# Kernel optimization log

Hardware: AMD Instinct MI355X
Metric: run time of the kernel (lower is better)

## Reference

```python
import jax, jax.numpy as jnp
import numpy as np

N = 100000      # nodes
E = 1600000     # edges (avg degree 16)
DIN = 128       # in_feats
H = 4           # num_heads
D = 32          # out_feats per head
NEG_SLOPE = 0.2


def setup_inputs() -> dict:
    key = jax.random.key(0)
    k1, k2, k3, k4, k5, k6 = jax.random.split(key, 6)
    feat = jax.random.normal(k1, (N, DIN), dtype=jnp.float32)
    src = jax.random.randint(k2, (E,), 0, N, dtype=jnp.int32)
    dst = jax.random.randint(k3, (E,), 0, N, dtype=jnp.int32)
    # learned params (fc kernel + attention vectors)
    W = jax.random.normal(k4, (DIN, H * D), dtype=jnp.float32) * 0.05
    attn_l = jax.random.normal(k5, (H, D), dtype=jnp.float32) * 0.05
    attn_r = jax.random.normal(k6, (H, D), dtype=jnp.float32) * 0.05
    return {"feat": feat, "src": src, "dst": dst, "W": W,
            "attn_l": attn_l, "attn_r": attn_r}


def reference(feat, src, dst, W, attn_l, attn_r):
    # linear projection: (N, DIN) @ (DIN, H*D) -> (N, H, D)
    h = (feat @ W).reshape(N, H, D)
    # per-node attention half-logits: (N, H)
    el = jnp.einsum("nhd,hd->nh", h, attn_l)
    er = jnp.einsum("nhd,hd->nh", h, attn_r)
    # edge-wise logits e_ij = LeakyReLU(el[src] + er[dst]) : (E, H)
    e = jax.nn.leaky_relu(el[src] + er[dst], negative_slope=NEG_SLOPE)
    # segment softmax over incoming edges of each dst node
    emax = jax.ops.segment_max(e, dst, num_segments=N)          # (N, H)
    emax = jnp.where(jnp.isfinite(emax), emax, 0.0)             # empty segs
    ee = jnp.exp(e - emax[dst])                                 # (E, H)
    denom = jax.ops.segment_sum(ee, dst, num_segments=N)        # (N, H)
    a = ee / denom[dst]                                         # (E, H)
    # weighted message + scatter-sum aggregation: (N, H, D)
    msg = h[src] * a[:, :, None]                                # (E, H, D)
    out = jax.ops.segment_sum(msg, dst, num_segments=N)
    return out
```

## Files before the change

kernel.cpp:

```cpp
#include <hip/hip_runtime.h>
#include <hip/hip_fp16.h>

#define N_NODES 100000
#define N_EDGES 1600000
#define DIN 128
#define NH 4
#define ND 32
#define HD 128
#define NEG_SLOPE 0.2f
#define MROWS 64
#define APAD 136
#define GEMM_BLOCKS ((N_NODES + MROWS - 1) / MROWS)

#define NBUCK 782
#define CHB 6400
#define NHB 250
#define WCONV_BLOCKS 64

typedef _Float16 half8_t __attribute__((ext_vector_type(8)));
typedef float f32x4 __attribute__((ext_vector_type(4)));

__device__ __forceinline__ float lrelu(float x) {
    return x > 0.0f ? x : NEG_SLOPE * x;
}

union Pack8  { uint2 u; __half2 h2[2]; };
union Pack16 { uint4 u; __half2 h2[4]; };

__global__ __launch_bounds__(256) void k_histw(
    const int* __restrict__ dst, int* __restrict__ hist,
    const float* __restrict__ W, __half* __restrict__ Wt) {
    __shared__ int cnt[NBUCK];
    const int tid = threadIdx.x;

    if ((int)blockIdx.x >= NHB) {
        int i = (blockIdx.x - NHB) * 256 + tid;
        int k = i >> 7, c = i & 127;
        Wt[c * DIN + k] = __float2half(W[k * HD + c]);
        return;
    }
    if (!hist) return;
    for (int i = tid; i < NBUCK; i += 256) cnt[i] = 0;
    __syncthreads();
    int base = blockIdx.x * CHB;
#pragma unroll
    for (int j = 0; j < CHB / 256; ++j) {
        int e = base + j * 256 + tid;
        if (e < N_EDGES) atomicAdd(&cnt[dst[e] >> 7], 1);
    }
    __syncthreads();
    int* hrow = hist + (size_t)blockIdx.x * NBUCK;
    for (int i = tid; i < NBUCK; i += 256) hrow[i] = cnt[i];
}

__global__ __launch_bounds__(256) void k_scanH(int* __restrict__ hist,
                                               int* __restrict__ tot) {
    __shared__ int wtot[4];
    int b = blockIdx.x, tid = threadIdx.x;
    int v = (tid < NHB) ? hist[(size_t)tid * NBUCK + b] : 0;
    int lane = tid & 63, wv = tid >> 6;
    int incl = v;
#pragma unroll
    for (int off = 1; off < 64; off <<= 1) {
        int t = __shfl_up(incl, off, 64);
        if (lane >= off) incl += t;
    }
    if (lane == 63) wtot[wv] = incl;
    __syncthreads();
    int woff = 0;
    for (int w = 0; w < wv; ++w) woff += wtot[w];
    if (tid < NHB) hist[(size_t)tid * NBUCK + b] = woff + incl - v;
    if (tid == 0) tot[b] = wtot[0] + wtot[1] + wtot[2] + wtot[3];
}

__global__ __launch_bounds__(256) void k_scanT(const int* __restrict__ tot,
                                               int* __restrict__ bucket_base,
                                               int* __restrict__ rowptr) {
    __shared__ int wtot[4];
    int tid = threadIdx.x;
    int idx0 = tid * 4;
    int v[4];
#pragma unroll
    for (int j = 0; j < 4; ++j) {
        int b = idx0 + j;
        v[j] = (b < NBUCK) ? tot[b] : 0;
    }
    int s = v[0] + v[1] + v[2] + v[3];
    int lane = tid & 63;
    int incl = s;
#pragma unroll
    for (int off = 1; off < 64; off <<= 1) {
        int t = __shfl_up(incl, off, 64);
        if (lane >= off) incl += t;
    }
    if (lane == 63) wtot[tid >> 6] = incl;
    __syncthreads();
    int woff = 0;
    for (int w = 0; w < (tid >> 6); ++w) woff += wtot[w];
    int run = woff + incl - s;
#pragma unroll
    for (int j = 0; j < 4; ++j) {
        int b = idx0 + j;
        if (b < NBUCK) {
            int old = v[j];
            bucket_base[b] = run;
            run += old;
        }
    }
    if (tid == 0) {
        int total = wtot[0] + wtot[1] + wtot[2] + wtot[3];
        bucket_base[NBUCK] = total;
        rowptr[N_NODES] = total;
    }
}

__global__ __launch_bounds__(256) void k_gemmcscat(
    const float* __restrict__ feat, const __half* __restrict__ Wt,
    const float* __restrict__ attn_l, const float* __restrict__ attn_r,
    __half* __restrict__ hhalf, float* __restrict__ el, float* __restrict__ er,
    const int* __restrict__ src, const int* __restrict__ dst,
    const int* __restrict__ hist, const int* __restrict__ bucket_base,
    int* __restrict__ bucketed) {

    __shared__ __align__(16) __half As[MROWS * APAD];
    __shared__ __align__(16) __half Bs[HD * APAD];

    const int tid = threadIdx.x;

    if ((int)blockIdx.x < NHB) {
        if (!bucketed) return;
        int* cur = (int*)As;
        const int* hrow = hist + (size_t)blockIdx.x * NBUCK;
        for (int i = tid; i < NBUCK; i += 256) cur[i] = bucket_base[i] + hrow[i];
        __syncthreads();
        int base = blockIdx.x * CHB;
#pragma unroll
        for (int j = 0; j < CHB / 256; ++j) {
            int e = base + j * 256 + tid;
            if (e < N_EDGES) {
                int d = dst[e];
                int slot = atomicAdd(&cur[d >> 7], 1);
                bucketed[slot] = src[e] | ((d & 127) << 17);
            }
        }
        return;
    }

    const int row0 = (blockIdx.x - NHB) * MROWS;

    {
        const uint4* Wv = (const uint4*)Wt;
#pragma unroll
        for (int i = 0; i < 8; ++i) {
            int idx = tid + i * 256;
            int c = idx >> 4, k8 = idx & 15;
            *(uint4*)(&Bs[c * APAD + k8 * 8]) = Wv[idx];
        }
    }
    {
#pragma unroll
        for (int i = 0; i < 8; ++i) {
            int idx = tid + i * 256;
            int r = idx >> 5, c4 = idx & 31;
            int row = row0 + r;
            float4 f = (row < N_NODES)
                ? *(const float4*)(feat + (size_t)row * DIN + c4 * 4)
                : make_float4(0.0f, 0.0f, 0.0f, 0.0f);
            Pack8 pk;
            pk.h2[0] = __floats2half2_rn(f.x, f.y);
            pk.h2[1] = __floats2half2_rn(f.z, f.w);
            *(uint2*)(&As[r * APAD + c4 * 4]) = pk.u;
        }
    }
    __syncthreads();

    const int l = tid & 63;
    const int wv = tid >> 6;
    const int lrow = l & 15;
    const int kid = l >> 4;

    f32x4 acc[8];
#pragma unroll
    for (int n = 0; n < 8; ++n) acc[n] = (f32x4){0.0f, 0.0f, 0.0f, 0.0f};

#pragma unroll
    for (int kb = 0; kb < 4; ++kb) {
        half8_t a = *(const half8_t*)(&As[(wv * 16 + lrow) * APAD + kb * 32 + kid * 8]);
#pragma unroll
        for (int n = 0; n < 8; ++n) {
            half8_t b = *(const half8_t*)(&Bs[(n * 16 + lrow) * APAD + kb * 32 + kid * 8]);
            acc[n] = __builtin_amdgcn_mfma_f32_16x16x32_f16(a, b, acc[n], 0, 0, 0);
        }
    }

    __syncthreads();
#pragma unroll
    for (int n = 0; n < 8; ++n)
#pragma unroll
        for (int r = 0; r < 4; ++r)
            As[(wv * 16 + kid * 4 + r) * APAD + n * 16 + lrow] =
                __float2half(acc[n][r]);
    __syncthreads();

    {
        int lr = tid >> 2;
        int row = row0 + lr;
        int head = tid & 3;
        if (row < N_NODES) {
            float suml = 0.0f, sumr = 0.0f;
#pragma unroll
            for (int q = 0; q < 4; ++q) {
                Pack16 p;
                p.u = *(const uint4*)(&As[lr * APAD + head * 32 + q * 8]);
                float4 al0 = *(const float4*)(attn_l + head * 32 + q * 8);
                float4 al1 = *(const float4*)(attn_l + head * 32 + q * 8 + 4);
                float4 ar0 = *(const float4*)(attn_r + head * 32 + q * 8);
                float4 ar1 = *(const float4*)(attn_r + head * 32 + q * 8 + 4);
                float2 x0 = __half22float2(p.h2[0]);
                float2 x1 = __half22float2(p.h2[1]);
                float2 x2 = __half22float2(p.h2[2]);
                float2 x3 = __half22float2(p.h2[3]);
                suml += x0.x * al0.x + x0.y * al0.y + x1.x * al0.z + x1.y * al0.w;
                suml += x2.x * al1.x + x2.y * al1.y + x3.x * al1.z + x3.y * al1.w;
                sumr += x0.x * ar0.x + x0.y * ar0.y + x1.x * ar0.z + x1.y * ar0.w;
                sumr += x2.x * ar1.x + x2.y * ar1.y + x3.x * ar1.z + x3.y * ar1.w;
                *(uint4*)(hhalf + (size_t)row * HD + head * 32 + q * 8) = p.u;
            }
            el[(size_t)row * NH + head] = suml;
            er[(size_t)row * NH + head] = sumr;
        }
    }
}

__global__ __launch_bounds__(512) void k_fine(
    const int* __restrict__ bucketed, const int* __restrict__ bbase,
    int* __restrict__ srcs, int* __restrict__ rowptr) {

    __shared__ int cnt[128];
    __shared__ int noff[129];
    __shared__ int cur[128];

    const int b = blockIdx.x;
    const int tid = threadIdx.x;
    const int node0 = b << 7;
    const int beg = bbase[b], end = bbase[b + 1];

    if (tid < 128) cnt[tid] = 0;
    __syncthreads();

    for (int e = beg + tid; e < end; e += 512)
        atomicAdd(&cnt[bucketed[e] >> 17], 1);
    __syncthreads();

    if (tid < 64) {
        int v0 = cnt[tid * 2], v1 = cnt[tid * 2 + 1];
        int s = v0 + v1;
        int incl = s;
#pragma unroll
        for (int off = 1; off < 64; off <<= 1) {
            int t = __shfl_up(incl, off, 64);
            if (tid >= off) incl += t;
        }
        int excl = incl - s;
        noff[tid * 2] = excl;
        noff[tid * 2 + 1] = excl + v0;
        cur[tid * 2] = excl;
        cur[tid * 2 + 1] = excl + v0;
        if (tid == 63) noff[128] = incl;
    }
    __syncthreads();

    if (tid < 128) {
        int node = node0 + tid;
        if (node < N_NODES) rowptr[node] = beg + noff[tid];
    }

    for (int e = beg + tid; e < end; e += 512) {
        int p = bucketed[e];
        int d7 = p >> 17;
        int slot = beg + atomicAdd(&cur[d7], 1);
        srcs[slot] = p & 0x1FFFF;
    }
}

__global__ __launch_bounds__(256) void k_agg_csr(
    const int* __restrict__ rowptr, const int* __restrict__ srcs,
    const float* __restrict__ el, const float* __restrict__ er,
    const __half* __restrict__ hhalf, float* __restrict__ out) {
    int node = blockIdx.x * 4 + (threadIdx.x >> 6);
    int lane = threadIdx.x & 63;
    int grp = lane >> 4;
    int cl = lane & 15;
    int head = cl >> 2;
    int beg = rowptr[node], end = rowptr[node + 1];

    const float er_h = er[(size_t)node * NH + head];

    float dsum = 0.0f;
    float a[8];
#pragma unroll
    for (int q = 0; q < 8; ++q) a[q] = 0.0f;

    int i = beg + grp;
    for (; i + 12 < end; i += 16) {
        int s0 = srcs[i], s1 = srcs[i + 4], s2 = srcs[i + 8], s3 = srcs[i + 12];
        float e0 = el[(size_t)s0 * NH + head];
        float e1 = el[(size_t)s1 * NH + head];
        float e2 = el[(size_t)s2 * NH + head];
        float e3 = el[(size_t)s3 * NH + head];
        Pack16 p0, p1, p2, p3;
        p0.u = *(const uint4*)(hhalf + (size_t)s0 * HD + cl * 8);
        p1.u = *(const uint4*)(hhalf + (size_t)s1 * HD + cl * 8);
        p2.u = *(const uint4*)(hhalf + (size_t)s2 * HD + cl * 8);
        p3.u = *(const uint4*)(hhalf + (size_t)s3 * HD + cl * 8);
        float w0 = __expf(lrelu(e0 + er_h));
        float w1 = __expf(lrelu(e1 + er_h));
        float w2 = __expf(lrelu(e2 + er_h));
        float w3 = __expf(lrelu(e3 + er_h));
        dsum += (w0 + w1) + (w2 + w3);
#pragma unroll
        for (int q = 0; q < 4; ++q) {
            float2 x0 = __half22float2(p0.h2[q]);
            float2 x1 = __half22float2(p1.h2[q]);
            float2 x2 = __half22float2(p2.h2[q]);
            float2 x3 = __half22float2(p3.h2[q]);
            a[2 * q]     = fmaf(x0.x, w0, a[2 * q]);
            a[2 * q + 1] = fmaf(x0.y, w0, a[2 * q + 1]);
            a[2 * q]     = fmaf(x1.x, w1, a[2 * q]);
            a[2 * q + 1] = fmaf(x1.y, w1, a[2 * q + 1]);
            a[2 * q]     = fmaf(x2.x, w2, a[2 * q]);
            a[2 * q + 1] = fmaf(x2.y, w2, a[2 * q + 1]);
            a[2 * q]     = fmaf(x3.x, w3, a[2 * q]);
            a[2 * q + 1] = fmaf(x3.y, w3, a[2 * q + 1]);
        }
    }
    for (; i + 4 < end; i += 8) {
        int s0 = srcs[i], s1 = srcs[i + 4];
        float e0 = el[(size_t)s0 * NH + head];
        float e1 = el[(size_t)s1 * NH + head];
        Pack16 p0, p1;
        p0.u = *(const uint4*)(hhalf + (size_t)s0 * HD + cl * 8);
        p1.u = *(const uint4*)(hhalf + (size_t)s1 * HD + cl * 8);
        float w0 = __expf(lrelu(e0 + er_h));
        float w1 = __expf(lrelu(e1 + er_h));
        dsum += w0 + w1;
#pragma unroll
        for (int q = 0; q < 4; ++q) {
            float2 x0 = __half22float2(p0.h2[q]);
            float2 x1 = __half22float2(p1.h2[q]);
            a[2 * q]     = fmaf(x0.x, w0, a[2 * q]);
            a[2 * q + 1] = fmaf(x0.y, w0, a[2 * q + 1]);
            a[2 * q]     = fmaf(x1.x, w1, a[2 * q]);
            a[2 * q + 1] = fmaf(x1.y, w1, a[2 * q + 1]);
        }
    }
    if (i < end) {
        int s0 = srcs[i];
        float w0 = __expf(lrelu(el[(size_t)s0 * NH + head] + er_h));
        Pack16 p0;
        p0.u = *(const uint4*)(hhalf + (size_t)s0 * HD + cl * 8);
        dsum += w0;
#pragma unroll
        for (int q = 0; q < 4; ++q) {
            float2 x0 = __half22float2(p0.h2[q]);
            a[2 * q]     = fmaf(x0.x, w0, a[2 * q]);
            a[2 * q + 1] = fmaf(x0.y, w0, a[2 * q + 1]);
        }
    }

    dsum += __shfl_xor(dsum, 16, 64);
    dsum += __shfl_xor(dsum, 32, 64);
#pragma unroll
    for (int q = 0; q < 8; ++q) {
        a[q] += __shfl_xor(a[q], 16, 64);
        a[q] += __shfl_xor(a[q], 32, 64);
    }

    if (grp == 0) {
        float inv = (end > beg) ? 1.0f / dsum : 0.0f;
        *(float4*)(out + (size_t)node * HD + cl * 8) =
            make_float4(a[0] * inv, a[1] * inv, a[2] * inv, a[3] * inv);
        *(float4*)(out + (size_t)node * HD + cl * 8 + 4) =
            make_float4(a[4] * inv, a[5] * inv, a[6] * inv, a[7] * inv);
    }
}

__global__ void k_init_fb(float* __restrict__ out, float* __restrict__ denom) {
    int i = blockIdx.x * blockDim.x + threadIdx.x;
    int stride = gridDim.x * blockDim.x;
    for (int j = i; j < N_NODES * HD; j += stride) out[j] = 0.0f;
    for (int j = i; j < N_NODES * NH; j += stride) denom[j] = 0.0f;
}

__global__ __launch_bounds__(256) void k_denom_fb(
    const int* __restrict__ src, const int* __restrict__ dst,
    const float* __restrict__ el, const float* __restrict__ er,
    float* __restrict__ denom) {
    int e = blockIdx.x * blockDim.x + threadIdx.x;
    if (e >= N_EDGES) return;
    int s = src[e], d = dst[e];
    float4 l = *(const float4*)(el + (size_t)s * NH);
    float4 r = *(const float4*)(er + (size_t)d * NH);
    float* dn = denom + (size_t)d * NH;
    atomicAdd(dn + 0, __expf(lrelu(l.x + r.x)));
    atomicAdd(dn + 1, __expf(lrelu(l.y + r.y)));
    atomicAdd(dn + 2, __expf(lrelu(l.z + r.z)));
    atomicAdd(dn + 3, __expf(lrelu(l.w + r.w)));
}

__global__ __launch_bounds__(256) void k_agg_fb(
    const int* __restrict__ src, const int* __restrict__ dst,
    const float* __restrict__ el, const float* __restrict__ er,
    const float* __restrict__ denom, const __half* __restrict__ hhalf,
    float* __restrict__ out) {
    long long t = (long long)blockIdx.x * blockDim.x + threadIdx.x;
    if (t >= (long long)N_EDGES * HD) return;
    int e = (int)(t >> 7);
    int c = (int)(t & 127);
    int hh = c >> 5;
    int s = src[e], d = dst[e];
    float x = lrelu(el[(size_t)s * NH + hh] + er[(size_t)d * NH + hh]);
    float a = __expf(x) / denom[(size_t)d * NH + hh];
    atomicAdd(out + (size_t)d * HD + c,
              __half2float(hhalf[(size_t)s * HD + c]) * a);
}

extern "C" void kernel_launch(void* const* d_in, const int* in_sizes, int n_in,
                              void* d_out, int out_size, void* d_ws, size_t ws_size,
                              hipStream_t stream) {
    const float* feat   = (const float*)d_in[0];
    const int*   src    = (const int*)d_in[1];
    const int*   dst    = (const int*)d_in[2];
    const float* W      = (const float*)d_in[3];
    const float* attn_l = (const float*)d_in[4];
    const float* attn_r = (const float*)d_in[5];
    float* out = (float*)d_out;

    char* base = (char*)d_ws;
    size_t off = 0;
    auto take = [&](size_t bytes) -> char* {
        char* r = base + off;
        off = (off + bytes + 255) & ~(size_t)255;
        return r;
    };
    __half* hhalf  = (__half*)take((size_t)N_NODES * HD * 2);
    float* el      = (float*)take((size_t)N_NODES * NH * 4);
    float* er      = (float*)take((size_t)N_NODES * NH * 4);
    __half* Wt     = (__half*)take((size_t)DIN * HD * 2);
    int*  hist     = (int*)take((size_t)NHB * NBUCK * 4);
    int*  tot      = (int*)take((size_t)NBUCK * 4);
    int*  bbase    = (int*)take((size_t)(NBUCK + 1) * 4);
    int*  bucketed = (int*)take((size_t)N_EDGES * 4);
    int*  srcs     = (int*)take((size_t)N_EDGES * 4);
    int*  rowptr   = (int*)take((size_t)(N_NODES + 1) * 4);
    float* denom   = (float*)take((size_t)N_NODES * NH * 4);
    bool csr = (off <= ws_size);

    if (csr) {
        k_histw<<<NHB + WCONV_BLOCKS, 256, 0, stream>>>(dst, hist, W, Wt);
        k_scanH<<<NBUCK, 256, 0, stream>>>(hist, tot);
        k_scanT<<<1, 256, 0, stream>>>(tot, bbase, rowptr);
        k_gemmcscat<<<NHB + GEMM_BLOCKS, 256, 0, stream>>>(
            feat, Wt, attn_l, attn_r, hhalf, el, er,
            src, dst, hist, bbase, bucketed);
        k_fine<<<NBUCK, 512, 0, stream>>>(bucketed, bbase, srcs, rowptr);
        k_agg_csr<<<N_NODES / 4, 256, 0, stream>>>(rowptr, srcs, el, er,
                                                   hhalf, out);
    } else {
        int eb = (N_EDGES + 255) / 256;
        k_init_fb<<<2048, 256, 0, stream>>>(out, denom);
        k_histw<<<NHB + WCONV_BLOCKS, 256, 0, stream>>>(dst, (int*)nullptr,
                                                        W, Wt);
        k_gemmcscat<<<NHB + GEMM_BLOCKS, 256, 0, stream>>>(
            feat, Wt, attn_l, attn_r, hhalf, el, er,
            src, dst, (const int*)nullptr, (const int*)nullptr, (int*)nullptr);
        k_denom_fb<<<eb, 256, 0, stream>>>(src, dst, el, er, denom);
        long long totw = (long long)N_EDGES * HD;
        int ab = (int)((totw + 255) / 256);
        k_agg_fb<<<ab, 256, 0, stream>>>(src, dst, el, er, denom, hhalf, out);
    }
}
```

Measured before the change: 147.0 us.

## Split GEMM tiles across scatter and fine-sort kernels to overlap work

Moves the projection GEMM tile code into a shared device function and splits the GEMM blocks between two launches. The first 800 tiles run alongside the coarse bucket scatter, and the remaining tiles run in a new fused kernel alongside the fine per-node sort, whose blocks shrink from 512 to 256 threads. The aim is to balance the load and fill the GPU in both phases instead of running a GEMM-heavy kernel followed by a lighter sort kernel. The risk is that 256-thread sort blocks run more slowly, and the shared-memory footprint of the fused kernel could reduce occupancy.

```diff
diff --git a/kernel.cpp b/kernel.cpp
--- a/kernel.cpp
+++ b/kernel.cpp
@@ -11,6 +11,7 @@
 #define MROWS 64
 #define APAD 136
 #define GEMM_BLOCKS ((N_NODES + MROWS - 1) / MROWS)
+#define G1SPLIT 800
 
 #define NBUCK 782
 #define CHB 6400
@@ -27,126 +28,11 @@
 union Pack8  { uint2 u; __half2 h2[2]; };
 union Pack16 { uint4 u; __half2 h2[4]; };
 
-__global__ __launch_bounds__(256) void k_histw(
-    const int* __restrict__ dst, int* __restrict__ hist,
-    const float* __restrict__ W, __half* __restrict__ Wt) {
-    __shared__ int cnt[NBUCK];
-    const int tid = threadIdx.x;
-
-    if ((int)blockIdx.x >= NHB) {
-        int i = (blockIdx.x - NHB) * 256 + tid;
-        int k = i >> 7, c = i & 127;
-        Wt[c * DIN + k] = __float2half(W[k * HD + c]);
-        return;
-    }
-    if (!hist) return;
-    for (int i = tid; i < NBUCK; i += 256) cnt[i] = 0;
-    __syncthreads();
-    int base = blockIdx.x * CHB;
-#pragma unroll
-    for (int j = 0; j < CHB / 256; ++j) {
-        int e = base + j * 256 + tid;
-        if (e < N_EDGES) atomicAdd(&cnt[dst[e] >> 7], 1);
-    }
-    __syncthreads();
-    int* hrow = hist + (size_t)blockIdx.x * NBUCK;
-    for (int i = tid; i < NBUCK; i += 256) hrow[i] = cnt[i];
-}
-
-__global__ __launch_bounds__(256) void k_scanH(int* __restrict__ hist,
-                                               int* __restrict__ tot) {
-    __shared__ int wtot[4];
-    int b = blockIdx.x, tid = threadIdx.x;
-    int v = (tid < NHB) ? hist[(size_t)tid * NBUCK + b] : 0;
-    int lane = tid & 63, wv = tid >> 6;
-    int incl = v;
-#pragma unroll
-    for (int off = 1; off < 64; off <<= 1) {
-        int t = __shfl_up(incl, off, 64);
-        if (lane >= off) incl += t;
-    }
-    if (lane == 63) wtot[wv] = incl;
-    __syncthreads();
-    int woff = 0;
-    for (int w = 0; w < wv; ++w) woff += wtot[w];
-    if (tid < NHB) hist[(size_t)tid * NBUCK + b] = woff + incl - v;
-    if (tid == 0) tot[b] = wtot[0] + wtot[1] + wtot[2] + wtot[3];
-}
-
-__global__ __launch_bounds__(256) void k_scanT(const int* __restrict__ tot,
-                                               int* __restrict__ bucket_base,
-                                               int* __restrict__ rowptr) {
-    __shared__ int wtot[4];
-    int tid = threadIdx.x;
-    int idx0 = tid * 4;
-    int v[4];
-#pragma unroll
-    for (int j = 0; j < 4; ++j) {
-        int b = idx0 + j;
-        v[j] = (b < NBUCK) ? tot[b] : 0;
-    }
-    int s = v[0] + v[1] + v[2] + v[3];
-    int lane = tid & 63;
-    int incl = s;
-#pragma unroll
-    for (int off = 1; off < 64; off <<= 1) {
-        int t = __shfl_up(incl, off, 64);
-        if (lane >= off) incl += t;
-    }
-    if (lane == 63) wtot[tid >> 6] = incl;
-    __syncthreads();
-    int woff = 0;
-    for (int w = 0; w < (tid >> 6); ++w) woff += wtot[w];
-    int run = woff + incl - s;
-#pragma unroll
-    for (int j = 0; j < 4; ++j) {
-        int b = idx0 + j;
-        if (b < NBUCK) {
-            int old = v[j];
-            bucket_base[b] = run;
-            run += old;
-        }
-    }
-    if (tid == 0) {
-        int total = wtot[0] + wtot[1] + wtot[2] + wtot[3];
-        bucket_base[NBUCK] = total;
-        rowptr[N_NODES] = total;
-    }
-}
-
-__global__ __launch_bounds__(256) void k_gemmcscat(
-    const float* __restrict__ feat, const __half* __restrict__ Wt,
+__device__ __forceinline__ void gemm_tile(
+    int row0, const float* __restrict__ feat, const __half* __restrict__ Wt,
     const float* __restrict__ attn_l, const float* __restrict__ attn_r,
     __half* __restrict__ hhalf, float* __restrict__ el, float* __restrict__ er,
-    const int* __restrict__ src, const int* __restrict__ dst,
-    const int* __restrict__ hist, const int* __restrict__ bucket_base,
-    int* __restrict__ bucketed) {
-
-    __shared__ __align__(16) __half As[MROWS * APAD];
-    __shared__ __align__(16) __half Bs[HD * APAD];
-
-    const int tid = threadIdx.x;
-
-    if ((int)blockIdx.x < NHB) {
-        if (!bucketed) return;
-        int* cur = (int*)As;
-        const int* hrow = hist + (size_t)blockIdx.x * NBUCK;
-        for (int i = tid; i < NBUCK; i += 256) cur[i] = bucket_base[i] + hrow[i];
-        __syncthreads();
-        int base = blockIdx.x * CHB;
-#pragma unroll
-        for (int j = 0; j < CHB / 256; ++j) {
-            int e = base + j * 256 + tid;
-            if (e < N_EDGES) {
-                int d = dst[e];
-                int slot = atomicAdd(&cur[d >> 7], 1);
-                bucketed[slot] = src[e] | ((d & 127) << 17);
-            }
-        }
-        return;
-    }
-
-    const int row0 = (blockIdx.x - NHB) * MROWS;
+    __half* As, __half* Bs, int tid) {
 
     {
         const uint4* Wv = (const uint4*)Wt;
@@ -232,55 +118,191 @@
     }
 }
 
-__global__ __launch_bounds__(512) void k_fine(
+__global__ __launch_bounds__(256) void k_histw(
+    const int* __restrict__ dst, int* __restrict__ hist,
+    const float* __restrict__ W, __half* __restrict__ Wt) {
+    __shared__ int cnt[NBUCK];
+    const int tid = threadIdx.x;
+
+    if ((int)blockIdx.x >= NHB) {
+        int i = (blockIdx.x - NHB) * 256 + tid;
+        int k = i >> 7, c = i & 127;
+        Wt[c * DIN + k] = __float2half(W[k * HD + c]);
+        return;
+    }
+    if (!hist) return;
+    for (int i = tid; i < NBUCK; i += 256) cnt[i] = 0;
+    __syncthreads();
+    int base = blockIdx.x * CHB;
+#pragma unroll
+    for (int j = 0; j < CHB / 256; ++j) {
+        int e = base + j * 256 + tid;
+        if (e < N_EDGES) atomicAdd(&cnt[dst[e] >> 7], 1);
+    }
+    __syncthreads();
+    int* hrow = hist + (size_t)blockIdx.x * NBUCK;
+    for (int i = tid; i < NBUCK; i += 256) hrow[i] = cnt[i];
+}
+
+__global__ __launch_bounds__(256) void k_scanH(int* __restrict__ hist,
+                                               int* __restrict__ tot) {
+    __shared__ int wtot[4];
+    int b = blockIdx.x, tid = threadIdx.x;
+    int v = (tid < NHB) ? hist[(size_t)tid * NBUCK + b] : 0;
+    int lane = tid & 63, wv = tid >> 6;
+    int incl = v;
+#pragma unroll
+    for (int off = 1; off < 64; off <<= 1) {
+        int t = __shfl_up(incl, off, 64);
+        if (lane >= off) incl += t;
+    }
+    if (lane == 63) wtot[wv] = incl;
+    __syncthreads();
+    int woff = 0;
+    for (int w = 0; w < wv; ++w) woff += wtot[w];
+    if (tid < NHB) hist[(size_t)tid * NBUCK + b] = woff + incl - v;
+    if (tid == 0) tot[b] = wtot[0] + wtot[1] + wtot[2] + wtot[3];
+}
+
+__global__ __launch_bounds__(256) void k_scanT(const int* __restrict__ tot,
+                                               int* __restrict__ bucket_base,
+                                               int* __restrict__ rowptr) {
+    __shared__ int wtot[4];
+    int tid = threadIdx.x;
+    int idx0 = tid * 4;
+    int v[4];
+#pragma unroll
+    for (int j = 0; j < 4; ++j) {
+        int b = idx0 + j;
+        v[j] = (b < NBUCK) ? tot[b] : 0;
+    }
+    int s = v[0] + v[1] + v[2] + v[3];
+    int lane = tid & 63;
+    int incl = s;
+#pragma unroll
+    for (int off = 1; off < 64; off <<= 1) {
+        int t = __shfl_up(incl, off, 64);
+        if (lane >= off) incl += t;
+    }
+    if (lane == 63) wtot[tid >> 6] = incl;
+    __syncthreads();
+    int woff = 0;
+    for (int w = 0; w < (tid >> 6); ++w) woff += wtot[w];
+    int run = woff + incl - s;
+#pragma unroll
+    for (int j = 0; j < 4; ++j) {
+        int b = idx0 + j;
+        if (b < NBUCK) {
+            int old = v[j];
+            bucket_base[b] = run;
+            run += old;
+        }
+    }
+    if (tid == 0) {
+        int total = wtot[0] + wtot[1] + wtot[2] + wtot[3];
+        bucket_base[NBUCK] = total;
+        rowptr[N_NODES] = total;
+    }
+}
+
+__global__ __launch_bounds__(256) void k_gemmcscat(
+    const float* __restrict__ feat, const __half* __restrict__ Wt,
+    const float* __restrict__ attn_l, const float* __restrict__ attn_r,
+    __half* __restrict__ hhalf, float* __restrict__ el, float* __restrict__ er,
+    const int* __restrict__ src, const int* __restrict__ dst,
+    const int* __restrict__ hist, const int* __restrict__ bucket_base,
+    int* __restrict__ bucketed) {
+
+    __shared__ __align__(16) __half As[MROWS * APAD];
+    __shared__ __align__(16) __half Bs[HD * APAD];
+
+    const int tid = threadIdx.x;
+
+    if ((int)blockIdx.x < NHB) {
+        if (!bucketed) return;
+        int* cur = (int*)As;
+        const int* hrow = hist + (size_t)blockIdx.x * NBUCK;
+        for (int i = tid; i < NBUCK; i += 256) cur[i] = bucket_base[i] + hrow[i];
+        __syncthreads();
+        int base = blockIdx.x * CHB;
+#pragma unroll
+        for (int j = 0; j < CHB / 256; ++j) {
+            int e = base + j * 256 + tid;
+            if (e < N_EDGES) {
+                int d = dst[e];
+                int slot = atomicAdd(&cur[d >> 7], 1);
+                bucketed[slot] = src[e] | ((d & 127) << 17);
+            }
+        }
+        return;
+    }
+
+    gemm_tile((blockIdx.x - NHB) * MROWS, feat, Wt, attn_l, attn_r,
+              hhalf, el, er, As, Bs, tid);
+}
+
+__global__ __launch_bounds__(256) void k_gemmfine(
+    const float* __restrict__ feat, const __half* __restrict__ Wt,
+    const float* __restrict__ attn_l, const float* __restrict__ attn_r,
+    __half* __restrict__ hhalf, float* __restrict__ el, float* __restrict__ er,
     const int* __restrict__ bucketed, const int* __restrict__ bbase,
     int* __restrict__ srcs, int* __restrict__ rowptr) {
 
-    __shared__ int cnt[128];
-    __shared__ int noff[129];
-    __shared__ int cur[128];
-
-    const int b = blockIdx.x;
+    __shared__ __align__(16) __half As[MROWS * APAD];
+    __shared__ __align__(16) __half Bs[HD * APAD];
+
     const int tid = threadIdx.x;
-    const int node0 = b << 7;
-    const int beg = bbase[b], end = bbase[b + 1];
-
-    if (tid < 128) cnt[tid] = 0;
-    __syncthreads();
-
-    for (int e = beg + tid; e < end; e += 512)
-        atomicAdd(&cnt[bucketed[e] >> 17], 1);
-    __syncthreads();
-
-    if (tid < 64) {
-        int v0 = cnt[tid * 2], v1 = cnt[tid * 2 + 1];
-        int s = v0 + v1;
-        int incl = s;
-#pragma unroll
-        for (int off = 1; off < 64; off <<= 1) {
-            int t = __shfl_up(incl, off, 64);
-            if (tid >= off) incl += t;
-        }
-        int excl = incl - s;
-        noff[tid * 2] = excl;
-        noff[tid * 2 + 1] = excl + v0;
-        cur[tid * 2] = excl;
-        cur[tid * 2 + 1] = excl + v0;
-        if (tid == 63) noff[128] = incl;
-    }
-    __syncthreads();
-
-    if (tid < 128) {
-        int node = node0 + tid;
-        if (node < N_NODES) rowptr[node] = beg + noff[tid];
-    }
-
-    for (int e = beg + tid; e < end; e += 512) {
-        int p = bucketed[e];
-        int d7 = p >> 17;
-        int slot = beg + atomicAdd(&cur[d7], 1);
-        srcs[slot] = p & 0x1FFFF;
-    }
+
+    if ((int)blockIdx.x < NBUCK) {
+        int* cnt  = (int*)As;
+        int* noff = cnt + 128;
+        int* cur  = noff + 129;
+
+        const int b = blockIdx.x;
+        const int node0 = b << 7;
+        const int beg = bbase[b], end = bbase[b + 1];
+
+        if (tid < 128) cnt[tid] = 0;
+        __syncthreads();
+
+        for (int e = beg + tid; e < end; e += 256)
+            atomicAdd(&cnt[bucketed[e] >> 17], 1);
+        __syncthreads();
+
+        if (tid < 64) {
+            int v0 = cnt[tid * 2], v1 = cnt[tid * 2 + 1];
+            int s = v0 + v1;
+            int incl = s;
+#pragma unroll
+            for (int off = 1; off < 64; off <<= 1) {
+                int t = __shfl_up(incl, off, 64);
+                if (tid >= off) incl += t;
+            }
+            int excl = incl - s;
+            noff[tid * 2] = excl;
+            noff[tid * 2 + 1] = excl + v0;
+            cur[tid * 2] = excl;
+            cur[tid * 2 + 1] = excl + v0;
+            if (tid == 63) noff[128] = incl;
+        }
+        __syncthreads();
+
+        if (tid < 128) {
+            int node = node0 + tid;
+            if (node < N_NODES) rowptr[node] = beg + noff[tid];
+        }
+
+        for (int e = beg + tid; e < end; e += 256) {
+            int p = bucketed[e];
+            int d7 = p >> 17;
+            int slot = beg + atomicAdd(&cur[d7], 1);
+            srcs[slot] = p & 0x1FFFF;
+        }
+        return;
+    }
+
+    gemm_tile((blockIdx.x - NBUCK + G1SPLIT) * MROWS, feat, Wt, attn_l, attn_r,
+              hhalf, el, er, As, Bs, tid);
 }
 
 __global__ __launch_bounds__(256) void k_agg_csr(
@@ -460,10 +482,12 @@
         k_histw<<<NHB + WCONV_BLOCKS, 256, 0, stream>>>(dst, hist, W, Wt);
         k_scanH<<<NBUCK, 256, 0, stream>>>(hist, tot);
         k_scanT<<<1, 256, 0, stream>>>(tot, bbase, rowptr);
-        k_gemmcscat<<<NHB + GEMM_BLOCKS, 256, 0, stream>>>(
+        k_gemmcscat<<<NHB + G1SPLIT, 256, 0, stream>>>(
             feat, Wt, attn_l, attn_r, hhalf, el, er,
             src, dst, hist, bbase, bucketed);
-        k_fine<<<NBUCK, 512, 0, stream>>>(bucketed, bbase, srcs, rowptr);
+        k_gemmfine<<<NBUCK + (GEMM_BLOCKS - G1SPLIT), 256, 0, stream>>>(
+            feat, Wt, attn_l, attn_r, hhalf, el, er,
+            bucketed, bbase, srcs, rowptr);
         k_agg_csr<<<N_NODES / 4, 256, 0, stream>>>(rowptr, srcs, el, er,
                                                    hhalf, out);
     } else {
```

After: 151.2 us. 1.03x slower.
